# Performance work log

Measured on AMD Instinct MI355X. Metric: run time of the kernel, lower is better.

Reference implementation:

```python
import jax, jax.numpy as jnp
import numpy as np

NQ, NS, QN, SN = 10000, 500, 4, 10   # num_question, num_skill, q/s neighbor sizes
B, S, D = 32, 200, 128               # batch, seq_len, emb_dim
HOPS = 3


def setup_inputs() -> dict:
    key = jax.random.key(0)
    ks = iter(jax.random.split(key, 40))

    def nrm(shape, scale=0.05):
        return jax.random.normal(next(ks), shape, dtype=jnp.float32) * scale

    return {
        "question": jax.random.randint(next(ks), (B, S), 0, NQ),
        "response": jax.random.randint(next(ks), (B, S), 0, 2),
        "mask": jnp.ones((B, S), dtype=jnp.int32),
        "q_neighbors": jax.random.randint(next(ks), (NQ, QN), 0, NS),  # question -> skill ids
        "s_neighbors": jax.random.randint(next(ks), (NS, SN), 0, NQ),  # skill -> question ids
        "qs_skills": jax.random.randint(next(ks), (NQ, 4), 0, NS),     # related skills per question
        "emb_q": nrm((NQ, D), 1.0),
        "emb_s": nrm((NS, D), 1.0),
        "emb_r": nrm((2, D), 1.0),
        "W_ih": nrm((2 * D, 4 * D)), "b_ih": nrm((4 * D,)), "b_hh": nrm((4 * D,)),
        "ft_W": nrm((D, D)), "ft_b": nrm((D,)),
        "agg_W": nrm((HOPS, D, D)), "agg_b": nrm((HOPS, D)),
        "last_W": nrm((D, D)), "last_b": nrm((D,)),
        "q_W": nrm((D, D)), "q_b": nrm((D,)),
        "k_W": nrm((D, D)), "k_b": nrm((D,)),
        "w_W": nrm((2 * D,)), "w_b": nrm(()),
    }


def reference(question, response, mask, q_neighbors, s_neighbors, qs_skills,
              emb_q, emb_s, emb_r, W_ih, b_ih, b_hh, ft_W, ft_b,
              agg_W, agg_b, last_W, last_b, q_W, q_b, k_W, k_b, w_W, w_b):
    # ---- multi-hop GNN aggregation for every (b, t) question (mask == 1 everywhere) ----
    q_flat = question.reshape(-1)              # [B*S]
    lvl1 = q_neighbors[q_flat]                 # [N, QN]            skill ids
    lvl2 = s_neighbors[lvl1]                   # [N, QN, SN]        question ids
    lvl3 = q_neighbors[lvl2]                   # [N, QN, SN, QN]    skill ids
    embs = [emb_q[q_flat], emb_s[lvl1], emb_q[lvl2], emb_s[lvl3]]
    for i in range(HOPS):
        embs = [jnp.tanh((embs[j] + embs[j + 1].mean(axis=-2)) @ agg_W[j] + agg_b[j])
                for j in range(HOPS - i)]
    agg_emb = jnp.tanh(embs[0] @ last_W + last_b).reshape(B, S, D)

    # ---- per-step input + zero-state LSTMCell (source calls lstm_cell without hx) ----
    q_trans = jax.nn.relu(agg_emb @ ft_W + ft_b)
    x = jnp.concatenate([q_trans, emb_r[response]], axis=-1)   # [B, S, 2D]
    gates = x @ W_ih + b_ih + b_hh                             # h_prev = 0, c_prev = 0
    i_g, f_g, g_g, o_g = jnp.split(gates, 4, axis=-1)
    c = jax.nn.sigmoid(i_g) * jnp.tanh(g_g)
    h = jax.nn.sigmoid(o_g) * jnp.tanh(c)                      # [B, S, D]
    states = h[:, :S - 1]                                      # state written at step t

    # ---- soft-recap attention prediction for q_next = question[:, t+1] ----
    q_next = question[:, 1:]                                   # [B, T], T = S-1
    qs = jnp.concatenate([emb_q[q_next][:, :, None, :], emb_s[qs_skills[q_next]]], axis=2)  # [B,T,5,D]

    inner = jnp.einsum('bnd,btmd->btnm', states, qs)           # state/qs inner products
    a_state = (states @ q_W + q_b) @ w_W[:D]                   # [B, N]  MLP_query on states
    a_qs = (qs @ k_W + k_b) @ w_W[D:]                          # [B, T, 5] MLP_key on qs
    logits = a_state[:, None, :, None] + a_qs[:, :, None, :] + w_b  # [B, T, N, 5]

    t_idx = jnp.arange(S - 1)
    valid = t_idx[None, :] <= t_idx[:, None]                   # [T, N]: states 0..t visible at t
    logits = jnp.where(valid[None, :, :, None], logits, -jnp.inf)
    alpha = jax.nn.softmax(logits.reshape(B, S - 1, -1), axis=-1).reshape(logits.shape)
    pred = jnp.sum(alpha * jax.nn.sigmoid(inner), axis=(2, 3))  # [B, T]

    return jnp.zeros((B, S), jnp.float32).at[:, 1:].set(pred)
```

## Files before the change

kernel.cpp:

```cpp
#include <hip/hip_runtime.h>

typedef unsigned short u16;
typedef unsigned int   u32;

#define NQd 10000
#define NSd 500
#define Bd  32
#define Sd  200
#define Td  199
#define Dd  128
#define NR  6368
#define PB  208

typedef __attribute__((ext_vector_type(8))) short bf16x8;
typedef __attribute__((ext_vector_type(4))) float f32x4;

__device__ __forceinline__ float sigf(float x) {
  return __builtin_amdgcn_rcpf(1.f + __expf(-x));
}
__device__ __forceinline__ float tanh_f(float x) {
  float ax = fminf(fabsf(x), 15.f);
  float e = __expf(2.f * ax);
  float r = 1.f - 2.f * __builtin_amdgcn_rcpf(e + 1.f);
  return copysignf(r, x);
}
__device__ __forceinline__ float bf2f(u16 u) { return __uint_as_float(((u32)u) << 16); }
__device__ __forceinline__ u16 f2bf(float f) {
  u32 b = __float_as_uint(f);
  b += 0x7FFFu + ((b >> 16) & 1u);
  return (u16)(b >> 16);
}
__device__ __forceinline__ float rnd(float x) { return bf2f(f2bf(x)); }
__device__ __forceinline__ void unp2(u32 u, float &a, float &b) {
  a = __uint_as_float(u << 16);
  b = __uint_as_float(u & 0xffff0000u);
}
__device__ __forceinline__ void unpack16(uint4 a0, uint4 a1, float* f) {
  unp2(a0.x, f[0], f[1]);  unp2(a0.y, f[2], f[3]);
  unp2(a0.z, f[4], f[5]);  unp2(a0.w, f[6], f[7]);
  unp2(a1.x, f[8], f[9]);  unp2(a1.y, f[10], f[11]);
  unp2(a1.z, f[12], f[13]); unp2(a1.w, f[14], f[15]);
}

struct Args {
  const int *question, *response, *q_nb, *s_nb, *qs_sk;
  const float *emb_q, *emb_s, *emb_r;
  const float *W_ih, *b_ih, *b_hh, *ft_W, *ft_b, *agg_W, *agg_b, *last_W, *last_b;
  const float *q_W, *q_b, *k_W, *k_b, *w_W;
  u16 *tabA, *tabB, *tabs1, *tabs2, *states, *embq_bf, *embs_bf, *wts, *wiht;
  float *a_state, *qw, *kw, *scal, *er_part, *ev, *invZ, *pm;
  int *qid_map, *resp_map, *flag, *cnt, *list, *newidx;
};

struct WF { bf16x8 v[2][4]; };

__device__ __forceinline__ void load_WF(const u16* Wt, int l15, int quad, int cw, WF& w)
{
#pragma unroll
  for (int nt = 0; nt < 2; ++nt)
#pragma unroll
    for (int kc = 0; kc < 4; ++kc)
      w.v[nt][kc] = *(const bf16x8*)&Wt[(long)(cw + nt * 16 + l15) * 128 + kc * 32 + quad * 8];
}

__device__ __forceinline__ void load_WF_f32(const float* W, int l15, int quad, int cw, WF& w)
{
#pragma unroll
  for (int nt = 0; nt < 2; ++nt) {
    int col = cw + nt * 16 + l15;
#pragma unroll
    for (int kc = 0; kc < 4; ++kc) {
      int kb = kc * 32 + quad * 8;
      bf16x8 t;
#pragma unroll
      for (int j = 0; j < 8; ++j) t[j] = (short)f2bf(W[(long)(kb + j) * 128 + col]);
      w.v[nt][kc] = t;
    }
  }
}

__device__ __forceinline__ void zero_acc(f32x4 acc[2][2]) {
#pragma unroll
  for (int x = 0; x < 2; ++x)
#pragma unroll
    for (int y = 0; y < 2; ++y) acc[x][y] = (f32x4){0.f, 0.f, 0.f, 0.f};
}

__device__ __forceinline__ void mfma_WF(const u16* Al, const WF& w,
                                        int l15, int quad, f32x4 acc[2][2])
{
#pragma unroll
  for (int kc = 0; kc < 4; ++kc) {
    const int ko = kc * 32 + quad * 8;
    bf16x8 a0 = *(const bf16x8*)&Al[l15 * 136 + ko];
    bf16x8 a1 = *(const bf16x8*)&Al[(16 + l15) * 136 + ko];
    acc[0][0] = __builtin_amdgcn_mfma_f32_16x16x32_bf16(a0, w.v[0][kc], acc[0][0], 0, 0, 0);
    acc[0][1] = __builtin_amdgcn_mfma_f32_16x16x32_bf16(a0, w.v[1][kc], acc[0][1], 0, 0, 0);
    acc[1][0] = __builtin_amdgcn_mfma_f32_16x16x32_bf16(a1, w.v[0][kc], acc[1][0], 0, 0, 0);
    acc[1][1] = __builtin_amdgcn_mfma_f32_16x16x32_bf16(a1, w.v[1][kc], acc[1][1], 0, 0, 0);
  }
}

__device__ __forceinline__ void stage_A(const u16* Atab, const u16* Btab,
                                        const int* nbr, int K, const int* rowmap,
                                        int tile0, int rows, int tid, u16* Al)
{
  int r = tid & 31, k0 = (tid >> 5) * 16;
  int row = tile0 + r; if (row >= rows) row = rows - 1;
  int arow = rowmap ? rowmap[row] : row;
  const u16* ap = Atab + (long)arow * 128 + k0;
  if (K == 0) {
    *(uint4*)&Al[r * 136 + k0]     = *(const uint4*)ap;
    *(uint4*)&Al[r * 136 + k0 + 8] = *(const uint4*)(ap + 8);
  } else {
    float f[16];
    unpack16(*(const uint4*)ap, *(const uint4*)(ap + 8), f);
    float s[16];
#pragma unroll
    for (int q = 0; q < 16; ++q) s[q] = 0.f;
    for (int l = 0; l < K; ++l) {
      int id = nbr[(long)arow * K + l];
      const u16* np = Btab + (long)id * 128 + k0;
      float g[16];
      unpack16(*(const uint4*)np, *(const uint4*)(np + 8), g);
#pragma unroll
      for (int q = 0; q < 16; ++q) s[q] += g[q];
    }
    float inv = 1.f / (float)K;
#pragma unroll
    for (int q = 0; q < 16; ++q) f[q] += s[q] * inv;
    u32 p[8];
#pragma unroll
    for (int q = 0; q < 8; ++q)
      p[q] = (u32)f2bf(f[2 * q]) | ((u32)f2bf(f[2 * q + 1]) << 16);
    *(uint4*)&Al[r * 136 + k0]     = make_uint4(p[0], p[1], p[2], p[3]);
    *(uint4*)&Al[r * 136 + k0 + 8] = make_uint4(p[4], p[5], p[6], p[7]);
  }
}

__device__ __forceinline__ void ld16_rnd(const float* p, float* f)
{
#pragma unroll
  for (int q4 = 0; q4 < 4; ++q4) {
    float4 v = *(const float4*)(p + q4 * 4);
    f[q4 * 4 + 0] = rnd(v.x); f[q4 * 4 + 1] = rnd(v.y);
    f[q4 * 4 + 2] = rnd(v.z); f[q4 * 4 + 3] = rnd(v.w);
  }
}

__device__ __forceinline__ void stage_A_f32(const float* Atab, const float* Btab,
                                            const int* nbr, int K,
                                            int tile0, int rows, int tid, u16* Al)
{
  int r = tid & 31, k0 = (tid >> 5) * 16;
  int row = tile0 + r; if (row >= rows) row = rows - 1;
  float f[16];
  ld16_rnd(Atab + (long)row * 128 + k0, f);
  float s[16];
#pragma unroll
  for (int q = 0; q < 16; ++q) s[q] = 0.f;
  for (int l = 0; l < K; ++l) {
    int id = nbr[(long)row * K + l];
    float g[16];
    ld16_rnd(Btab + (long)id * 128 + k0, g);
#pragma unroll
    for (int q = 0; q < 16; ++q) s[q] += g[q];
  }
  float inv = 1.f / (float)K;
#pragma unroll
  for (int q = 0; q < 16; ++q) f[q] += s[q] * inv;
  u32 p[8];
#pragma unroll
  for (int q = 0; q < 8; ++q)
    p[q] = (u32)f2bf(f[2 * q]) | ((u32)f2bf(f[2 * q + 1]) << 16);
  *(uint4*)&Al[r * 136 + k0]     = make_uint4(p[0], p[1], p[2], p[3]);
  *(uint4*)&Al[r * 136 + k0 + 8] = make_uint4(p[4], p[5], p[6], p[7]);
}

__device__ __forceinline__ void update_A(const u16* Btab, const int* nbr,
                                         const int* rowmap, int tile0, int rows,
                                         int tid, u16* Al)
{
  int r = tid & 31, k0 = (tid >> 5) * 16;
  int row = tile0 + r; if (row >= rows) row = rows - 1;
  int arow = rowmap ? rowmap[row] : row;
  float f[16];
  unpack16(*(const uint4*)&Al[r * 136 + k0], *(const uint4*)&Al[r * 136 + k0 + 8], f);
  float s[16];
#pragma unroll
  for (int q = 0; q < 16; ++q) s[q] = 0.f;
#pragma unroll
  for (int l = 0; l < 4; ++l) {
    int id = nbr[(long)arow * 4 + l];
    const u16* np = Btab + (long)id * 128 + k0;
    float g[16];
    unpack16(*(const uint4*)np, *(const uint4*)(np + 8), g);
#pragma unroll
    for (int q = 0; q < 16; ++q) s[q] += g[q];
  }
#pragma unroll
  for (int q = 0; q < 16; ++q) f[q] += s[q] * 0.25f;
  u32 p[8];
#pragma unroll
  for (int q = 0; q < 8; ++q)
    p[q] = (u32)f2bf(f[2 * q]) | ((u32)f2bf(f[2 * q + 1]) << 16);
  *(uint4*)&Al[r * 136 + k0]     = make_uint4(p[0], p[1], p[2], p[3]);
  *(uint4*)&Al[r * 136 + k0 + 8] = make_uint4(p[4], p[5], p[6], p[7]);
}

__device__ __forceinline__ void epi_tanh_global(const f32x4 acc[2][2], const float* cbias,
                                                u16* out, int rows, int tile0,
                                                int l15, int quad, int cw)
{
#pragma unroll
  for (int nt = 0; nt < 2; ++nt) {
    int col = cw + nt * 16 + l15;
    float cb = cbias[col];
#pragma unroll
    for (int mt = 0; mt < 2; ++mt) {
      int rbase = tile0 + mt * 16 + quad * 4;
#pragma unroll
      for (int i = 0; i < 4; ++i) {
        int row = rbase + i;
        if (row >= rows) continue;
        out[(long)row * 128 + col] = f2bf(tanh_f(acc[mt][nt][i] + cb));
      }
    }
  }
}

__device__ __forceinline__ void epi_tanh_lds(const f32x4 acc[2][2], const float* cbias,
                                             u16* Al, int l15, int quad, int cw)
{
#pragma unroll
  for (int nt = 0; nt < 2; ++nt) {
    int col = cw + nt * 16 + l15;
    float cb = cbias[col];
#pragma unroll
    for (int mt = 0; mt < 2; ++mt)
#pragma unroll
      for (int i = 0; i < 4; ++i) {
        int rL = mt * 16 + quad * 4 + i;
        Al[rL * 136 + col] = f2bf(tanh_f(acc[mt][nt][i] + cb));
      }
  }
}

__global__ __launch_bounds__(256) void prep2(Args a, float* __restrict__ out)
{
  __shared__ __align__(16) u16 Al[32 * 136];
  const int i = blockIdx.x, tid = threadIdx.x;
  const int lane = tid & 63, wv = tid >> 6;
  const int l15 = lane & 15, quad = lane >> 4, cw = wv * 32;

  if (i < 313) {
    const int tile0 = i * 32;
    WF w2, w0;
    load_WF_f32(a.agg_W + 2 * 16384, l15, quad, cw, w2);
    load_WF_f32(a.agg_W, l15, quad, cw, w0);
    stage_A_f32(a.emb_q, a.emb_s, a.q_nb, 4, tile0, NQd, tid, Al);
    __syncthreads();
    f32x4 acc[2][2];
    zero_acc(acc);
    mfma_WF(Al, w2, l15, quad, acc);
    epi_tanh_global(acc, a.agg_b + 256, a.tabA, NQd, tile0, l15, quad, cw);
    zero_acc(acc);
    mfma_WF(Al, w0, l15, quad, acc);
    epi_tanh_global(acc, a.agg_b, a.tabB, NQd, tile0, l15, quad, cw);
    return;
  }
  if (i < 329) {
    const int tile0 = (i - 313) * 32;
    WF w1;
    load_WF_f32(a.agg_W + 16384, l15, quad, cw, w1);
    stage_A_f32(a.emb_s, a.emb_q, a.s_nb, 10, tile0, NSd, tid, Al);
    __syncthreads();
    f32x4 acc[2][2];
    zero_acc(acc);
    mfma_WF(Al, w1, l15, quad, acc);
    epi_tanh_global(acc, a.agg_b + 128, a.tabs1, NSd, tile0, l15, quad, cw);
    return;
  }

  const int T = 640 * 256;
  for (int j = (i - 329) * 256 + tid; j < 497506; j += T) {
    if (j < 320000) {
      float4 v = *(const float4*)&a.emb_q[(long)j * 4];
      ((uint2*)a.embq_bf)[j] = make_uint2(
          (u32)f2bf(v.x) | ((u32)f2bf(v.y) << 16),
          (u32)f2bf(v.z) | ((u32)f2bf(v.w) << 16));
    } else if (j < 336000) {
      int c = j - 320000;
      float4 v = *(const float4*)&a.emb_s[(long)c * 4];
      ((uint2*)a.embs_bf)[c] = make_uint2(
          (u32)f2bf(v.x) | ((u32)f2bf(v.y) << 16),
          (u32)f2bf(v.z) | ((u32)f2bf(v.w) << 16));
    } else if (j < 417920) {
      int e = j - 336000;
      int seg = e >> 14, r = e & 16383;
      int col = r >> 7, k = r & 127;
      const float* src = (seg < 3) ? (a.agg_W + seg * 16384)
                                   : (seg == 3 ? a.last_W : a.ft_W);
      a.wts[e] = f2bf(src[k * 128 + col]);
    } else if (j < 483456) {
      int e = j - 417920;
      int col = e >> 7, k = e & 127;
      a.wiht[e] = f2bf(a.W_ih[k * 512 + col]);
    } else if (j < 489824) {
      int jj = j - 483456;
      int b = jj / Td, s = jj - b * Td;
      int qid = a.question[b * Sd + s];
      a.qid_map[jj]  = qid;
      a.resp_map[jj] = a.response[b * Sd + s];
      if (atomicExch(&a.flag[qid], 1) == 0) {
        int idx = atomicAdd(a.cnt, 1);
        a.list[idx] = qid;
        a.newidx[qid] = idx;
      }
    } else if (j < 491106) {
      int s = j - 489824;
      if (s < 128) {
        float acc = 0;
        for (int e = 0; e < 128; ++e) acc += a.q_W[s * 128 + e] * a.w_W[e];
        a.qw[s] = acc;
      } else if (s < 256) {
        int d = s - 128; float acc = 0;
        for (int e = 0; e < 128; ++e) acc += a.k_W[d * 128 + e] * a.w_W[128 + e];
        a.kw[d] = acc;
      } else if (s == 256) {
        float acc = 0;
        for (int e = 0; e < 128; ++e) acc += a.q_b[e] * a.w_W[e];
        a.scal[0] = acc;
      } else if (s == 257) {
        float acc = 0;
        for (int e = 0; e < 128; ++e) acc += a.k_b[e] * a.w_W[128 + e];
        a.scal[1] = acc;
      } else {
        int e2 = s - 258, rr = e2 >> 9, col = e2 & 511;
        float acc = a.b_ih[col] + a.b_hh[col];
        for (int d = 0; d < 128; ++d) acc += a.emb_r[rr * Dd + d] * a.W_ih[(128 + d) * 512 + col];
        a.er_part[rr * 512 + col] = acc;
      }
    } else {
      out[j - 491106] = 0.f;
    }
  }
}

__global__ __launch_bounds__(256) void g1k(Args a)
{
  __shared__ __align__(16) u16 Al[32 * 136];
  const int tid = threadIdx.x, tile0 = blockIdx.x * 32;
  const int lane = tid & 63, wv = tid >> 6;
  const int l15 = lane & 15, quad = lane >> 4, cw = wv * 32;
  WF w1; load_WF(a.wts + 16384, l15, quad, cw, w1);
  stage_A(a.tabs1, a.tabA, a.s_nb, 10, nullptr, tile0, NSd, tid, Al);
  __syncthreads();
  f32x4 acc[2][2];
  zero_acc(acc);
  mfma_WF(Al, w1, l15, quad, acc);
  epi_tanh_global(acc, a.agg_b + 128, a.tabs2, NSd, tile0, l15, quad, cw);
}

__global__ __launch_bounds__(256) void chain4(Args a)
{
  const int cnt = *a.cnt;
  const int tile0 = blockIdx.x * 32;
  if (tile0 >= cnt) return;
  __shared__ __align__(16) u16 Al[32 * 136];
  const int tid = threadIdx.x;
  const int lane = tid & 63, wv = tid >> 6;
  const int l15 = lane & 15, quad = lane >> 4, cw = wv * 32;
  WF w0, w3, w4;
  load_WF(a.wts, l15, quad, cw, w0);
  load_WF(a.wts + 3 * 16384, l15, quad, cw, w3);
  load_WF(a.wts + 4 * 16384, l15, quad, cw, w4);
  f32x4 acc[2][2];

  stage_A(a.tabB, a.tabs1, a.q_nb, 4, a.list, tile0, cnt, tid, Al);
  __syncthreads();
  zero_acc(acc);
  mfma_WF(Al, w0, l15, quad, acc);
  __syncthreads();
  epi_tanh_lds(acc, a.agg_b, Al, l15, quad, cw);
  __syncthreads();
  update_A(a.tabs2, a.q_nb, a.list, tile0, cnt, tid, Al);
  __syncthreads();
  zero_acc(acc);
  mfma_WF(Al, w0, l15, quad, acc);
  __syncthreads();
  epi_tanh_lds(acc, a.agg_b, Al, l15, quad, cw);
  __syncthreads();
  zero_acc(acc);
  mfma_WF(Al, w3, l15, quad, acc);
  __syncthreads();
  epi_tanh_lds(acc, a.last_b, Al, l15, quad, cw);
  __syncthreads();
  zero_acc(acc);
  mfma_WF(Al, w4, l15, quad, acc);
#pragma unroll
  for (int nt = 0; nt < 2; ++nt) {
    int col = cw + nt * 16 + l15;
    float cb = a.ft_b[col];
#pragma unroll
    for (int mt = 0; mt < 2; ++mt) {
      int rbase = tile0 + mt * 16 + quad * 4;
#pragma unroll
      for (int i = 0; i < 4; ++i) {
        int row = rbase + i;
        if (row >= cnt) continue;
        a.tabA[(long)row * 128 + col] = f2bf(fmaxf(acc[mt][nt][i] + cb, 0.f));
      }
    }
  }
}

__global__ __launch_bounds__(256) void gates_k(Args a)
{
  __shared__ __align__(16) u16 Al[32 * 136];
  __shared__ float hb[32 * 132];
  const int tid = threadIdx.x;
  const int lane = tid & 63, wv = tid >> 6;
  const int l15 = lane & 15, quad = lane >> 4, cw = wv * 32;

  if (blockIdx.x >= 199) {
    int item = (blockIdx.x - 199) * 256 + tid;
    if (item >= NR) return;
    int b = item / Td, t = item - b * Td;
    int qn = a.question[b * Sd + t + 1];
    float am[5];
#pragma unroll
    for (int m = 0; m < 5; ++m) {
      const u16* src = (m == 0) ? a.embq_bf + (long)qn * 128
                                : a.embs_bf + (long)a.qs_sk[qn * 4 + (m - 1)] * 128;
      float s = 0.f;
      for (int k = 0; k < 128; k += 8) {
        uint4 u = *(const uint4*)&src[k];
        float f[8];
        unp2(u.x, f[0], f[1]); unp2(u.y, f[2], f[3]);
        unp2(u.z, f[4], f[5]); unp2(u.w, f[6], f[7]);
#pragma unroll
        for (int q = 0; q < 8; ++q) s = fmaf(f[q], a.kw[k + q], s);
      }
      am[m] = s + a.scal[1];
    }
    float mx = am[0];
#pragma unroll
    for (int m = 1; m < 5; ++m) mx = fmaxf(mx, am[m]);
    float ex[5], z = 0.f;
#pragma unroll
    for (int m = 0; m < 5; ++m) { ex[m] = __expf(am[m] - mx); z += ex[m]; }
    float iz = __builtin_amdgcn_rcpf(z);
#pragma unroll
    for (int m = 0; m < 5; ++m) a.pm[((long)b * PB + t) * 5 + m] = ex[m] * iz;
    return;
  }

  const int tile0 = blockIdx.x * 32;
  WF wg0, wg1, wg2;
  load_WF(a.wiht, l15, quad, cw, wg0);
  load_WF(a.wiht + (long)256 * 128, l15, quad, cw, wg1);
  load_WF(a.wiht + (long)384 * 128, l15, quad, cw, wg2);
  {
    int r = tid & 31, k0 = (tid >> 5) * 16;
    int row = tile0 + r;
    int arow = a.newidx[a.qid_map[row]];
    const u16* ap = a.tabA + (long)arow * 128 + k0;
    *(uint4*)&Al[r * 136 + k0]     = *(const uint4*)ap;
    *(uint4*)&Al[r * 136 + k0 + 8] = *(const uint4*)(ap + 8);
  }
  __syncthreads();
  f32x4 acc[3][2][2];
  zero_acc(acc[0]); mfma_WF(Al, wg0, l15, quad, acc[0]);
  zero_acc(acc[1]); mfma_WF(Al, wg1, l15, quad, acc[1]);
  zero_acc(acc[2]); mfma_WF(Al, wg2, l15, quad, acc[2]);
#pragma unroll
  for (int nt = 0; nt < 2; ++nt) {
    int colL = cw + nt * 16 + l15;
#pragma unroll
    for (int mt = 0; mt < 2; ++mt) {
#pragma unroll
      for (int i = 0; i < 4; ++i) {
        int rL = mt * 16 + quad * 4 + i;
        int row = tile0 + rL;
        const float* rb = a.er_part + (long)a.resp_map[row] * 512;
        float iv = acc[0][mt][nt][i] + rb[colL];
        float gv = acc[1][mt][nt][i] + rb[256 + colL];
        float ov = acc[2][mt][nt][i] + rb[384 + colL];
        float c = sigf(iv) * tanh_f(gv);
        float h = sigf(ov) * tanh_f(c);
        a.states[(long)row * 128 + colL] = f2bf(h);
        hb[rL * 132 + colL] = h;
      }
    }
  }
  __syncthreads();
#pragma unroll
  for (int rr = 0; rr < 8; ++rr) {
    int rL = wv * 8 + rr;
    float p = hb[rL * 132 + lane] * a.qw[lane] + hb[rL * 132 + 64 + lane] * a.qw[64 + lane];
#pragma unroll
    for (int off = 32; off > 0; off >>= 1) p += __shfl_xor(p, off);
    if (lane == 0) a.a_state[tile0 + rL] = p + a.scal[0];
  }
}

__global__ __launch_bounds__(256) void bprep(Args a)
{
  __shared__ float red[256];
  __shared__ float evl[256];
  const int b = blockIdx.x, tid = threadIdx.x;
  float v = (tid < Td) ? a.a_state[b * Td + tid] : -1e30f;
  red[tid] = v; __syncthreads();
  for (int s = 128; s > 0; s >>= 1) { if (tid < s) red[tid] = fmaxf(red[tid], red[tid + s]); __syncthreads(); }
  float gmax = red[0];
  float e = (tid < Td) ? __expf(v - gmax) : 0.f;
  evl[tid] = e;
  if (tid < Td) a.ev[b * PB + tid] = e;
  __syncthreads();
  for (int off = 1; off < 256; off <<= 1) {
    float add = (tid >= off) ? evl[tid - off] : 0.f;
    __syncthreads();
    evl[tid] += add;
    __syncthreads();
  }
  if (tid < Td) a.invZ[b * PB + tid] = 1.f / evl[tid];
}

__global__ __launch_bounds__(256) void gk_pred(Args a, float* __restrict__ out)
{
  const int n0 = blockIdx.x * 32;
  const int c0 = blockIdx.y * 128;
  const int b  = blockIdx.z;
  int c_hi = c0 + 127; if (c_hi > 994) c_hi = 994;
  const int tmax = c_hi / 5, tmin = c0 / 5;
  if (n0 > tmax) return;

  __shared__ __align__(16) u16 smem[21760];
  __shared__ float predl[32];
  u16* Ql = smem;
  u16* Sl = smem + 17408;
  const int tid = threadIdx.x;
  if (tid < 32) predl[tid] = 0.f;
  {
    int r = tid & 31, k0 = (tid >> 5) * 16;
    int n = n0 + r; if (n > 198) n = 198;
    const u16* sp = a.states + ((long)b * Td + n) * 128 + k0;
    *(uint4*)&Sl[r * 136 + k0]     = *(const uint4*)sp;
    *(uint4*)&Sl[r * 136 + k0 + 8] = *(const uint4*)(sp + 8);
  }
  {
    int j = tid >> 1, k0 = (tid & 1) * 64;
    int col = c0 + j;
    uint4* dst = (uint4*)&Ql[j * 136 + k0];
    if (col < 995) {
      int t = col / 5, m = col - t * 5;
      int qn = a.question[b * Sd + t + 1];
      const u16* src = (m == 0) ? a.embq_bf + (long)qn * 128
                                : a.embs_bf + (long)a.qs_sk[qn * 4 + (m - 1)] * 128;
      src += k0;
#pragma unroll
      for (int q = 0; q < 8; ++q) dst[q] = ((const uint4*)src)[q];
    } else {
      uint4 z = make_uint4(0, 0, 0, 0);
#pragma unroll
      for (int q = 0; q < 8; ++q) dst[q] = z;
    }
  }
  __syncthreads();
  const int lane = tid & 63, wv = tid >> 6;
  const int l15 = lane & 15, quad = lane >> 4, cw = wv * 32;
  f32x4 acc[2][2];
  zero_acc(acc);
#pragma unroll
  for (int kc = 0; kc < 4; ++kc) {
    const int ko = kc * 32 + quad * 8;
    bf16x8 af[2], bfv[2];
    af[0]  = *(const bf16x8*)&Sl[l15 * 136 + ko];
    af[1]  = *(const bf16x8*)&Sl[(16 + l15) * 136 + ko];
    bfv[0] = *(const bf16x8*)&Ql[(cw + l15) * 136 + ko];
    bfv[1] = *(const bf16x8*)&Ql[(cw + 16 + l15) * 136 + ko];
#pragma unroll
    for (int mt = 0; mt < 2; ++mt)
#pragma unroll
      for (int nt = 0; nt < 2; ++nt)
        acc[mt][nt] = __builtin_amdgcn_mfma_f32_16x16x32_bf16(af[mt], bfv[nt], acc[mt][nt], 0, 0, 0);
  }

#pragma unroll
  for (int nt = 0; nt < 2; ++nt) {
    int col = c0 + cw + nt * 16 + l15;
    if (col >= 995) continue;
    int t = col / 5, m = col - t * 5;
    float pmv = a.pm[((long)b * PB + t) * 5 + m];
    float part = 0.f;
#pragma unroll
    for (int mt = 0; mt < 2; ++mt) {
      int nb = n0 + mt * 16 + quad * 4;
      if (nb > t) continue;
      float4 ev4 = *(const float4*)&a.ev[b * PB + nb];
      float evv[4] = {ev4.x, ev4.y, ev4.z, ev4.w};
#pragma unroll
      for (int i = 0; i < 4; ++i) {
        int n = nb + i;
        if (n > t || n > 198) continue;
        part += evv[i] * sigf(acc[mt][nt][i]);
      }
    }
    part *= pmv;
    if (part != 0.f) atomicAdd(&predl[t - tmin], part);
  }
  __syncthreads();
  const int tcnt = tmax - tmin + 1;
  if (tid < tcnt) {
    int t = tmin + tid;
    float pv = predl[tid];
    if (pv != 0.f)
      atomicAdd(&out[b * Sd + t + 1], pv * a.invZ[b * PB + t]);
  }
}

extern "C" void kernel_launch(void* const* d_in, const int* in_sizes, int n_in,
                              void* d_out, int out_size, void* d_ws, size_t ws_size,
                              hipStream_t stream)
{
  Args a;
  a.question = (const int*)d_in[0];
  a.response = (const int*)d_in[1];
  a.q_nb     = (const int*)d_in[3];
  a.s_nb     = (const int*)d_in[4];
  a.qs_sk    = (const int*)d_in[5];
  a.emb_q    = (const float*)d_in[6];
  a.emb_s    = (const float*)d_in[7];
  a.emb_r    = (const float*)d_in[8];
  a.W_ih     = (const float*)d_in[9];
  a.b_ih     = (const float*)d_in[10];
  a.b_hh     = (const float*)d_in[11];
  a.ft_W     = (const float*)d_in[12];
  a.ft_b     = (const float*)d_in[13];
  a.agg_W    = (const float*)d_in[14];
  a.agg_b    = (const float*)d_in[15];
  a.last_W   = (const float*)d_in[16];
  a.last_b   = (const float*)d_in[17];
  a.q_W      = (const float*)d_in[18];
  a.q_b      = (const float*)d_in[19];
  a.k_W      = (const float*)d_in[20];
  a.k_b      = (const float*)d_in[21];
  a.w_W      = (const float*)d_in[22];

  u16* wsu = (u16*)d_ws;
  const long NT = 1280000, ST = 64000, RT = (long)NR * Dd;
  a.tabA  = wsu;
  a.tabB  = a.tabA + NT;
  a.tabs1 = a.tabB + NT;
  a.tabs2 = a.tabs1 + ST;
  a.states  = a.tabs2 + ST;
  a.embq_bf = a.states + RT;
  a.embs_bf = a.embq_bf + NT;
  a.wts     = a.embs_bf + ST;
  a.wiht    = a.wts + 5 * 16384;
  float* fp = (float*)(a.wiht + 65536);
  a.a_state = fp;
  a.qw      = fp + 6368;
  a.kw      = fp + 6496;
  a.scal    = fp + 6624;
  a.er_part = fp + 6640;
  a.ev      = fp + 7664;
  a.invZ    = a.ev + 32 * PB;
  a.pm      = a.invZ + 32 * PB;
  a.qid_map  = (int*)(a.pm + 32 * PB * 5);
  a.resp_map = a.qid_map + NR;
  a.flag     = a.resp_map + NR;
  a.cnt      = a.flag + NQd;
  a.list     = a.cnt + 4;
  a.newidx   = a.list + NQd;

  float* out = (float*)d_out;

  hipMemsetAsync(a.flag, 0, (NQd + 4) * sizeof(int), stream);
  prep2<<<969, 256, 0, stream>>>(a, out);
  g1k<<<16, 256, 0, stream>>>(a);
  chain4<<<199, 256, 0, stream>>>(a);
  gates_k<<<224, 256, 0, stream>>>(a);
  bprep<<<Bd, 256, 0, stream>>>(a);
  gk_pred<<<dim3(7, 8, Bd), 256, 0, stream>>>(a, out);
}
```

Before: 186.4 us.

## Fuse softmax prefix prep into prediction kernel and compact triangular block grid

Removes the separate bprep kernel. Each gk_pred block now recomputes the per-batch max, the exp values and their prefix sums in shared memory, which saves one launch and the global ev/invZ buffers. The grid also changes from a 7x8xB layout, where many blocks exited early on the causal triangle, to 14 chunks per batch, each looping over several 32-row state tiles. The cost is redundant scan work in every block and uneven per-block work, since a chunk handles one to three tiles.

New measurement: 180.4 us. -3.2%, faster.

```diff
diff --git a/kernel.cpp b/kernel.cpp
--- a/kernel.cpp
+++ b/kernel.cpp
@@ -48,7 +48,7 @@
   const float *W_ih, *b_ih, *b_hh, *ft_W, *ft_b, *agg_W, *agg_b, *last_W, *last_b;
   const float *q_W, *q_b, *k_W, *k_b, *w_W;
   u16 *tabA, *tabB, *tabs1, *tabs2, *states, *embq_bf, *embs_bf, *wts, *wiht;
-  float *a_state, *qw, *kw, *scal, *er_part, *ev, *invZ, *pm;
+  float *a_state, *qw, *kw, *scal, *er_part, *pm;
   int *qid_map, *resp_map, *flag, *cnt, *list, *newidx;
 };
 
@@ -505,50 +505,41 @@
   }
 }
 
-__global__ __launch_bounds__(256) void bprep(Args a)
-{
-  __shared__ float red[256];
-  __shared__ float evl[256];
-  const int b = blockIdx.x, tid = threadIdx.x;
-  float v = (tid < Td) ? a.a_state[b * Td + tid] : -1e30f;
-  red[tid] = v; __syncthreads();
-  for (int s = 128; s > 0; s >>= 1) { if (tid < s) red[tid] = fmaxf(red[tid], red[tid + s]); __syncthreads(); }
-  float gmax = red[0];
-  float e = (tid < Td) ? __expf(v - gmax) : 0.f;
-  evl[tid] = e;
-  if (tid < Td) a.ev[b * PB + tid] = e;
-  __syncthreads();
-  for (int off = 1; off < 256; off <<= 1) {
-    float add = (tid >= off) ? evl[tid - off] : 0.f;
-    __syncthreads();
-    evl[tid] += add;
-    __syncthreads();
-  }
-  if (tid < Td) a.invZ[b * PB + tid] = 1.f / evl[tid];
-}
-
 __global__ __launch_bounds__(256) void gk_pred(Args a, float* __restrict__ out)
 {
-  const int n0 = blockIdx.x * 32;
-  const int c0 = blockIdx.y * 128;
-  const int b  = blockIdx.z;
+  static const int cys[14]   = {0,1,2,3,3,4,4,5,5,6,6,7,7,7};
+  static const int nx0s[14]  = {0,0,0,0,3,0,3,0,3,0,3,0,3,6};
+  static const int ncnts[14] = {1,2,3,3,1,3,1,3,2,3,3,3,3,1};
+  const int chunk = blockIdx.x, b = blockIdx.y;
+  const int cy = cys[chunk], nx0 = nx0s[chunk], ncnt = ncnts[chunk];
+  const int c0 = cy * 128;
   int c_hi = c0 + 127; if (c_hi > 994) c_hi = 994;
   const int tmax = c_hi / 5, tmin = c0 / 5;
-  if (n0 > tmax) return;
 
   __shared__ __align__(16) u16 smem[21760];
   __shared__ float predl[32];
+  __shared__ float evl[256];
+  __shared__ float scl[256];
   u16* Ql = smem;
   u16* Sl = smem + 17408;
   const int tid = threadIdx.x;
+
+  float v = (tid < Td) ? a.a_state[b * Td + tid] : -1e30f;
+  scl[tid] = v; __syncthreads();
+  for (int s = 128; s > 0; s >>= 1) { if (tid < s) scl[tid] = fmaxf(scl[tid], scl[tid + s]); __syncthreads(); }
+  float gmax = scl[0]; __syncthreads();
+  float e = (tid < Td) ? __expf(v - gmax) : 0.f;
+  evl[tid] = e;
+  scl[tid] = e;
   if (tid < 32) predl[tid] = 0.f;
-  {
-    int r = tid & 31, k0 = (tid >> 5) * 16;
-    int n = n0 + r; if (n > 198) n = 198;
-    const u16* sp = a.states + ((long)b * Td + n) * 128 + k0;
-    *(uint4*)&Sl[r * 136 + k0]     = *(const uint4*)sp;
-    *(uint4*)&Sl[r * 136 + k0 + 8] = *(const uint4*)(sp + 8);
-  }
+  __syncthreads();
+  for (int off = 1; off < 256; off <<= 1) {
+    float add = (tid >= off) ? scl[tid - off] : 0.f;
+    __syncthreads();
+    scl[tid] += add;
+    __syncthreads();
+  }
+
   {
     int j = tid >> 1, k0 = (tid & 1) * 64;
     int col = c0 + j;
@@ -567,48 +558,59 @@
       for (int q = 0; q < 8; ++q) dst[q] = z;
     }
   }
-  __syncthreads();
+
   const int lane = tid & 63, wv = tid >> 6;
   const int l15 = lane & 15, quad = lane >> 4, cw = wv * 32;
-  f32x4 acc[2][2];
-  zero_acc(acc);
-#pragma unroll
-  for (int kc = 0; kc < 4; ++kc) {
-    const int ko = kc * 32 + quad * 8;
-    bf16x8 af[2], bfv[2];
-    af[0]  = *(const bf16x8*)&Sl[l15 * 136 + ko];
-    af[1]  = *(const bf16x8*)&Sl[(16 + l15) * 136 + ko];
-    bfv[0] = *(const bf16x8*)&Ql[(cw + l15) * 136 + ko];
-    bfv[1] = *(const bf16x8*)&Ql[(cw + 16 + l15) * 136 + ko];
-#pragma unroll
-    for (int mt = 0; mt < 2; ++mt)
-#pragma unroll
-      for (int nt = 0; nt < 2; ++nt)
-        acc[mt][nt] = __builtin_amdgcn_mfma_f32_16x16x32_bf16(af[mt], bfv[nt], acc[mt][nt], 0, 0, 0);
-  }
-
-#pragma unroll
-  for (int nt = 0; nt < 2; ++nt) {
-    int col = c0 + cw + nt * 16 + l15;
-    if (col >= 995) continue;
-    int t = col / 5, m = col - t * 5;
-    float pmv = a.pm[((long)b * PB + t) * 5 + m];
-    float part = 0.f;
-#pragma unroll
-    for (int mt = 0; mt < 2; ++mt) {
-      int nb = n0 + mt * 16 + quad * 4;
-      if (nb > t) continue;
-      float4 ev4 = *(const float4*)&a.ev[b * PB + nb];
-      float evv[4] = {ev4.x, ev4.y, ev4.z, ev4.w};
-#pragma unroll
-      for (int i = 0; i < 4; ++i) {
-        int n = nb + i;
-        if (n > t || n > 198) continue;
-        part += evv[i] * sigf(acc[mt][nt][i]);
-      }
-    }
-    part *= pmv;
-    if (part != 0.f) atomicAdd(&predl[t - tmin], part);
+
+  for (int xi = 0; xi < ncnt; ++xi) {
+    const int n0 = (nx0 + xi) * 32;
+    __syncthreads();
+    {
+      int r = tid & 31, k0 = (tid >> 5) * 16;
+      int n = n0 + r; if (n > 198) n = 198;
+      const u16* sp = a.states + ((long)b * Td + n) * 128 + k0;
+      *(uint4*)&Sl[r * 136 + k0]     = *(const uint4*)sp;
+      *(uint4*)&Sl[r * 136 + k0 + 8] = *(const uint4*)(sp + 8);
+    }
+    __syncthreads();
+    f32x4 acc[2][2];
+    zero_acc(acc);
+#pragma unroll
+    for (int kc = 0; kc < 4; ++kc) {
+      const int ko = kc * 32 + quad * 8;
+      bf16x8 af[2], bfv[2];
+      af[0]  = *(const bf16x8*)&Sl[l15 * 136 + ko];
+      af[1]  = *(const bf16x8*)&Sl[(16 + l15) * 136 + ko];
+      bfv[0] = *(const bf16x8*)&Ql[(cw + l15) * 136 + ko];
+      bfv[1] = *(const bf16x8*)&Ql[(cw + 16 + l15) * 136 + ko];
+#pragma unroll
+      for (int mt = 0; mt < 2; ++mt)
+#pragma unroll
+        for (int nt = 0; nt < 2; ++nt)
+          acc[mt][nt] = __builtin_amdgcn_mfma_f32_16x16x32_bf16(af[mt], bfv[nt], acc[mt][nt], 0, 0, 0);
+    }
+
+#pragma unroll
+    for (int nt = 0; nt < 2; ++nt) {
+      int col = c0 + cw + nt * 16 + l15;
+      if (col >= 995) continue;
+      int t = col / 5, m = col - t * 5;
+      float pmv = a.pm[((long)b * PB + t) * 5 + m];
+      float part = 0.f;
+#pragma unroll
+      for (int mt = 0; mt < 2; ++mt) {
+        int nb = n0 + mt * 16 + quad * 4;
+        if (nb > t) continue;
+#pragma unroll
+        for (int i = 0; i < 4; ++i) {
+          int n = nb + i;
+          if (n > t || n > 198) continue;
+          part += evl[n] * sigf(acc[mt][nt][i]);
+        }
+      }
+      part *= pmv;
+      if (part != 0.f) atomicAdd(&predl[t - tmin], part);
+    }
   }
   __syncthreads();
   const int tcnt = tmax - tmin + 1;
@@ -616,7 +618,7 @@
     int t = tmin + tid;
     float pv = predl[tid];
     if (pv != 0.f)
-      atomicAdd(&out[b * Sd + t + 1], pv * a.invZ[b * PB + t]);
+      atomicAdd(&out[b * Sd + t + 1], pv * (1.f / scl[t]));
   }
 }
 
@@ -665,9 +667,7 @@
   a.kw      = fp + 6496;
   a.scal    = fp + 6624;
   a.er_part = fp + 6640;
-  a.ev      = fp + 7664;
-  a.invZ    = a.ev + 32 * PB;
-  a.pm      = a.invZ + 32 * PB;
+  a.pm      = fp + 7664;
   a.qid_map  = (int*)(a.pm + 32 * PB * 5);
   a.resp_map = a.qid_map + NR;
   a.flag     = a.resp_map + NR;
@@ -682,6 +682,5 @@
   g1k<<<16, 256, 0, stream>>>(a);
   chain4<<<199, 256, 0, stream>>>(a);
   gates_k<<<224, 256, 0, stream>>>(a);
-  bprep<<<Bd, 256, 0, stream>>>(a);
-  gk_pred<<<dim3(7, 8, Bd), 256, 0, stream>>>(a, out);
-}
+  gk_pred<<<dim3(14, Bd), 256, 0, stream>>>(a, out);
+}
```
